# Kernel tuning notes

Hardware: AMD Instinct MI355X
Metric: run time of the kernel (lower is better)

Reference implementation:

```python
import jax, jax.numpy as jnp
import numpy as np

DMODEL = 2048
HEADS = 16
DHEAD = DMODEL // HEADS  # 128


def setup_inputs() -> dict:
    key = jax.random.key(0)
    ks = jax.random.split(key, 9)
    s = 0.02
    x = jax.random.normal(ks[0], (4, 2048, DMODEL), dtype=jnp.float32)
    Wq = jax.random.normal(ks[1], (DMODEL, DMODEL), dtype=jnp.float32) * s
    bq = jax.random.normal(ks[2], (DMODEL,), dtype=jnp.float32) * s
    Wk = jax.random.normal(ks[3], (DMODEL, DMODEL), dtype=jnp.float32) * s
    bk = jax.random.normal(ks[4], (DMODEL,), dtype=jnp.float32) * s
    Wv = jax.random.normal(ks[5], (DMODEL, DMODEL), dtype=jnp.float32) * s
    bv = jax.random.normal(ks[6], (DMODEL,), dtype=jnp.float32) * s
    Wo = jax.random.normal(ks[7], (DMODEL, DMODEL), dtype=jnp.float32) * s
    bo = jax.random.normal(ks[8], (DMODEL,), dtype=jnp.float32) * s
    return {"x": x, "Wq": Wq, "bq": bq, "Wk": Wk, "bk": bk, "Wv": Wv, "bv": bv, "Wo": Wo, "bo": bo}


def reference(x, Wq, bq, Wk, bk, Wv, bv, Wo, bo):
    b, l, _ = x.shape
    # projections: [b, l, dmodel] -> [b, l, heads, dhead]
    q = (x @ Wq + bq).reshape(b, l, HEADS, DHEAD)
    k = (x @ Wk + bk).reshape(b, l, HEADS, DHEAD)
    v = (x @ Wv + bv).reshape(b, l, HEADS, DHEAD)
    # NOTE: source applies 1/sqrt(dhead) twice -> total scale 1/dhead (faithful)
    a = jnp.einsum('blhd,bLhd->bhlL', q, k) * (1.0 / DHEAD)
    a = jax.nn.softmax(a, axis=-1)
    prefinal = jnp.einsum('bhlL,bLhd->blhd', a, v)
    out = prefinal.reshape(b, l, HEADS * DHEAD) @ Wo + bo
    return out
```

## Files before the change

kernel.cpp:

```cpp
#include <hip/hip_runtime.h>

#define DMODEL 2048
#define SEQ    2048
#define BATCH  4
#define HEADS  16
#define DHEAD  128

typedef __attribute__((ext_vector_type(8))) short short8;
typedef __attribute__((ext_vector_type(4))) float f32x4;
typedef __attribute__((ext_vector_type(16))) float f32x16;

__device__ __forceinline__ unsigned short f2bf(float f) {
  union { float f; unsigned u; } v; v.f = f;
  unsigned r = v.u + 0x7FFFu + ((v.u >> 16) & 1u);
  return (unsigned short)(r >> 16);
}

__global__ __launch_bounds__(256) void cvt_f32_bf16(const float* __restrict__ in,
                                                    unsigned short* __restrict__ out,
                                                    int n4) {
  int i = blockIdx.x * 256 + threadIdx.x;
  if (i >= n4) return;
  float4 v = ((const float4*)in)[i];
  ushort4 o;
  o.x = f2bf(v.x); o.y = f2bf(v.y); o.z = f2bf(v.z); o.w = f2bf(v.w);
  ((ushort4*)out)[i] = o;
}

__global__ __launch_bounds__(256) void transpose_cvt(const float* __restrict__ in,
                                                     unsigned short* __restrict__ out) {
  __shared__ float tile[32][33];
  const int tx = threadIdx.x, ty = threadIdx.y;
  const int x = blockIdx.x * 32 + tx;
  const int y0 = blockIdx.y * 32;
#pragma unroll
  for (int j = 0; j < 32; j += 8)
    tile[ty + j][tx] = in[(size_t)(y0 + ty + j) * DMODEL + x];
  __syncthreads();
  const int xo = blockIdx.y * 32 + tx;
  const int yo0 = blockIdx.x * 32;
#pragma unroll
  for (int j = 0; j < 32; j += 8)
    out[(size_t)(yo0 + ty + j) * DMODEL + xo] = f2bf(tile[tx][ty + j]);
}

__global__ __launch_bounds__(256) void transpose_v(const unsigned short* __restrict__ in,
                                                   unsigned short* __restrict__ out) {
  __shared__ unsigned short t[32][33];
  const int tx = threadIdx.x, ty = threadIdx.y;
  const int bid = blockIdx.x;
  const int lb = bid & 63;
  const int db = (bid >> 6) & 3;
  const int h  = (bid >> 8) & 15;
  const int b  = bid >> 12;
#pragma unroll
  for (int j = 0; j < 32; j += 8)
    t[ty + j][tx] = in[(size_t)(b * SEQ + lb * 32 + ty + j) * DMODEL + h * DHEAD + db * 32 + tx];
  __syncthreads();
  const size_t ob = ((size_t)(b * HEADS + h) * DHEAD + db * 32) * SEQ + lb * 32;
#pragma unroll
  for (int j = 0; j < 32; j += 8)
    out[ob + (size_t)(ty + j) * SEQ + tx] = t[tx][ty + j];
}

template <typename OUT_T, int NTN>
__global__ __launch_bounds__(512, 2) void gemm2(const unsigned short* __restrict__ A,
                                                const unsigned short* __restrict__ Bt,
                                                const float* __restrict__ b0,
                                                const float* __restrict__ b1,
                                                const float* __restrict__ b2,
                                                OUT_T* __restrict__ C) {
  __shared__ unsigned short As[2][256 * 64];
  __shared__ unsigned short Bs[2][256 * 64];

  const int tid = threadIdx.x;
  const int l = tid & 63, w = tid >> 6;
  const int wr = w >> 2, wc = w & 3;

  const int bid = blockIdx.x;
  const int q8 = (32 * NTN) >> 3;
  const int swz = (bid & 7) * q8 + (bid >> 3);
  const int tn = swz % NTN;
  const int tm = swz / NTN;

  const int srow = w * 8 + (l >> 3);
  const int schunk = (l & 7) ^ (l >> 3);
  const unsigned short* Ag = A + (size_t)(tm * 256 + srow) * DMODEL + schunk * 8;
  const unsigned short* Bg = Bt + (size_t)(tn * 256 + srow) * DMODEL + schunk * 8;

#define GLL(src, dst) __builtin_amdgcn_global_load_lds( \
    (const __attribute__((address_space(1))) void*)(src), \
    (__attribute__((address_space(3))) void*)(dst), 16, 0, 0)

#define STAGE(bf, kt) do { \
    GLL(Ag + (size_t)0 * 64 * DMODEL + (kt) * 64,   &As[bf][0 * 4096 + w * 512]); \
    GLL(Ag + (size_t)1 * 64 * DMODEL + (kt) * 64,   &As[bf][1 * 4096 + w * 512]); \
    GLL(Ag + (size_t)2 * 64 * DMODEL + (kt) * 64,   &As[bf][2 * 4096 + w * 512]); \
    GLL(Ag + (size_t)3 * 64 * DMODEL + (kt) * 64,   &As[bf][3 * 4096 + w * 512]); \
    GLL(Bg + (size_t)0 * 64 * DMODEL + (kt) * 64,   &Bs[bf][0 * 4096 + w * 512]); \
    GLL(Bg + (size_t)1 * 64 * DMODEL + (kt) * 64,   &Bs[bf][1 * 4096 + w * 512]); \
    GLL(Bg + (size_t)2 * 64 * DMODEL + (kt) * 64,   &Bs[bf][2 * 4096 + w * 512]); \
    GLL(Bg + (size_t)3 * 64 * DMODEL + (kt) * 64,   &Bs[bf][3 * 4096 + w * 512]); \
  } while (0)

  f32x4 acc[8][4] = {};

  STAGE(0, 0);
  int buf = 0;
  for (int t = 0; t < 32; ++t) {
    __builtin_amdgcn_s_barrier();
    __builtin_amdgcn_sched_barrier(0);
    if (t < 31) {
      STAGE(buf ^ 1, t + 1);
      __builtin_amdgcn_sched_barrier(0);
      asm volatile("s_waitcnt vmcnt(8)" ::: "memory");
    } else {
      asm volatile("s_waitcnt vmcnt(0)" ::: "memory");
    }
    __builtin_amdgcn_sched_barrier(0);
    __builtin_amdgcn_s_barrier();
    __builtin_amdgcn_sched_barrier(0);

    {
      const unsigned short* Asb = &As[buf][0];
      const unsigned short* Bsb = &Bs[buf][0];
      short8 bfr[4][2];
#pragma unroll
      for (int n = 0; n < 4; ++n) {
        const int row = wc * 64 + n * 16 + (l & 15);
#pragma unroll
        for (int ks = 0; ks < 2; ++ks)
          bfr[n][ks] = *(const short8*)&Bsb[row * 64 + (((ks * 4 + (l >> 4)) ^ (row & 7)) * 8)];
      }
      __builtin_amdgcn_s_setprio(1);
#pragma unroll
      for (int m = 0; m < 8; ++m) {
        const int row = wr * 128 + m * 16 + (l & 15);
        short8 af0 = *(const short8*)&Asb[row * 64 + (((0 + (l >> 4)) ^ (row & 7)) * 8)];
        short8 af1 = *(const short8*)&Asb[row * 64 + (((4 + (l >> 4)) ^ (row & 7)) * 8)];
#pragma unroll
        for (int n = 0; n < 4; ++n) {
          acc[m][n] = __builtin_amdgcn_mfma_f32_16x16x32_bf16(af0, bfr[n][0], acc[m][n], 0, 0, 0);
          acc[m][n] = __builtin_amdgcn_mfma_f32_16x16x32_bf16(af1, bfr[n][1], acc[m][n], 0, 0, 0);
        }
      }
      __builtin_amdgcn_s_setprio(0);
    }
    buf ^= 1;
  }
#undef STAGE
#undef GLL

  const int bsel = tn >> 3;
  const float* bp = (bsel == 0) ? b0 : ((bsel == 1) ? b1 : b2);
  OUT_T* Cb = C + (size_t)bsel * ((size_t)8192 * DMODEL);
  const int row0 = tm * 256 + wr * 128 + ((l >> 4) * 4);
  const int lc0 = (tn & 7) * 256 + wc * 64 + (l & 15);
#pragma unroll
  for (int n = 0; n < 4; ++n) {
    float bv = bp[lc0 + n * 16];
#pragma unroll
    for (int m = 0; m < 8; ++m) {
#pragma unroll
      for (int r = 0; r < 4; ++r) {
        float v = acc[m][n][r] + bv;
        size_t idx = (size_t)(row0 + m * 16 + r) * DMODEL + (lc0 + n * 16);
        if constexpr (sizeof(OUT_T) == 2) ((unsigned short*)Cb)[idx] = f2bf(v);
        else                              ((float*)Cb)[idx] = v;
      }
    }
  }
}

__global__ __launch_bounds__(256) void attn(const unsigned short* __restrict__ Q,
                                            const unsigned short* __restrict__ K,
                                            const unsigned short* __restrict__ V,
                                            unsigned short* __restrict__ O) {
  __shared__ unsigned short Ks[32 * 136];
  __shared__ unsigned short Vt[128 * 40];
  __shared__ unsigned short Ps[4][16 * 40];

  const int tid = threadIdx.x;
  const int l = tid & 63, w = tid >> 6;
  const int bh = blockIdx.x >> 5, qb = blockIdx.x & 31;
  const int b = bh >> 4, h = bh & 15;
  const size_t base = ((size_t)b * SEQ) * DMODEL + (size_t)h * DHEAD;

  const unsigned short* Qp = Q + base + (size_t)(qb * 64 + w * 16) * DMODEL;
  short8 qf[4];
#pragma unroll
  for (int dc = 0; dc < 4; ++dc)
    qf[dc] = *(const short8*)(Qp + (size_t)(l & 15) * DMODEL + dc * 32 + (l >> 4) * 8);

  f32x4 acc[8] = {};
  float sum[4] = {0.f, 0.f, 0.f, 0.f};

  const int skv = tid >> 3;
  const int sc = (tid & 7) * 16;
  const unsigned short* Kg = K + base + (size_t)skv * DMODEL + sc;
  const unsigned short* Vg = V + base + (size_t)skv * DMODEL + sc;

  const float cexp = 1.4426950408889634f / 128.0f;

  for (int kv0 = 0; kv0 < SEQ; kv0 += 32) {
    __syncthreads();
    short8 ka = *(const short8*)(Kg + (size_t)kv0 * DMODEL);
    short8 kb = *(const short8*)(Kg + (size_t)kv0 * DMODEL + 8);
    *(short8*)&Ks[skv * 136 + sc] = ka;
    *(short8*)&Ks[skv * 136 + sc + 8] = kb;
    short8 va = *(const short8*)(Vg + (size_t)kv0 * DMODEL);
    short8 vb = *(const short8*)(Vg + (size_t)kv0 * DMODEL + 8);
#pragma unroll
    for (int j = 0; j < 8; ++j) {
      Vt[(sc + j) * 40 + skv]     = (unsigned short)va[j];
      Vt[(sc + 8 + j) * 40 + skv] = (unsigned short)vb[j];
    }
    __syncthreads();

    f32x4 s[2];
#pragma unroll
    for (int nh = 0; nh < 2; ++nh) {
      f32x4 t = {};
#pragma unroll
      for (int dc = 0; dc < 4; ++dc) {
        short8 kf = *(const short8*)&Ks[(nh * 16 + (l & 15)) * 136 + dc * 32 + (l >> 4) * 8];
        t = __builtin_amdgcn_mfma_f32_16x16x32_bf16(qf[dc], kf, t, 0, 0, 0);
      }
      s[nh] = t;
    }

#pragma unroll
    for (int nh = 0; nh < 2; ++nh) {
#pragma unroll
      for (int r = 0; r < 4; ++r) {
        float p = exp2f(s[nh][r] * cexp);
        sum[r] += p;
        Ps[w][((l >> 4) * 4 + r) * 40 + (l & 15) + nh * 16] = f2bf(p);
      }
    }

    short8 pf = *(const short8*)&Ps[w][(l & 15) * 40 + (l >> 4) * 8];
#pragma unroll
    for (int db = 0; db < 8; ++db) {
      short8 vf = *(const short8*)&Vt[(db * 16 + (l & 15)) * 40 + (l >> 4) * 8];
      acc[db] = __builtin_amdgcn_mfma_f32_16x16x32_bf16(pf, vf, acc[db], 0, 0, 0);
    }
  }

  float inv[4];
#pragma unroll
  for (int r = 0; r < 4; ++r) {
    float s = sum[r];
    s += __shfl_xor(s, 1);
    s += __shfl_xor(s, 2);
    s += __shfl_xor(s, 4);
    s += __shfl_xor(s, 8);
    inv[r] = 1.0f / s;
  }
  unsigned short* Op = O + base + (size_t)(qb * 64 + w * 16) * DMODEL;
#pragma unroll
  for (int db = 0; db < 8; ++db)
#pragma unroll
    for (int r = 0; r < 4; ++r)
      Op[(size_t)((l >> 4) * 4 + r) * DMODEL + db * 16 + (l & 15)] = f2bf(acc[db][r] * inv[r]);
}

__global__ __launch_bounds__(256, 2) void attn6(const unsigned short* __restrict__ Q,
                                                const unsigned short* __restrict__ K,
                                                const unsigned short* __restrict__ VT,
                                                unsigned short* __restrict__ O) {
  __shared__ unsigned short Ks[2][64 * 128];
  __shared__ unsigned short Vs[2][128 * 64];

  const int tid = threadIdx.x;
  const int l = tid & 63, w = tid >> 6;
  const int x32 = l & 31, h = l >> 5;

  const int bid = blockIdx.x;
  const int swz = (bid & 7) * 64 + (bid >> 3);
  const int bh = swz >> 3, qb = swz & 7;
  const int b = bh >> 4, hh = bh & 15;
  const size_t base = ((size_t)b * SEQ) * DMODEL + (size_t)hh * DHEAD;
  const unsigned short* VTb = VT + (size_t)bh * DHEAD * SEQ;

  const unsigned short* Qp = Q + base + (size_t)(qb * 256 + w * 64) * DMODEL;
  short8 qfA[8], qfB[8];
#pragma unroll
  for (int dc = 0; dc < 8; ++dc) {
    qfA[dc] = *(const short8*)(Qp + (size_t)x32 * DMODEL + dc * 16 + h * 8);
    qfB[dc] = *(const short8*)(Qp + (size_t)(x32 + 32) * DMODEL + dc * 16 + h * 8);
  }

  const unsigned short* Kg0 = K + base + (size_t)(w * 16 + (l >> 4)) * DMODEL + (((l & 15) ^ (l >> 4)) * 8);
  const unsigned short* Kg1 = K + base + (size_t)(w * 16 + (l >> 4)) * DMODEL + (((l & 15) ^ ((l >> 4) + 4)) * 8);
  const unsigned short* Vg0 = VTb + (size_t)(w * 32 + (l >> 3)) * SEQ + (((l & 7) ^ (l >> 3)) * 8);

  unsigned short* KsD = &Ks[0][0];
  unsigned short* VsD = &Vs[0][0];

#define GLL(src, dst) __builtin_amdgcn_global_load_lds( \
    (const __attribute__((address_space(1))) void*)(src), \
    (__attribute__((address_space(3))) void*)(dst), 16, 0, 0)

#define STAGE(bf, kv0) do { \
    GLL(Kg0 + (size_t)(kv0) * DMODEL,        KsD + (bf) * 8192 + w * 2048 + 0 * 512); \
    GLL(Kg1 + (size_t)((kv0) + 4) * DMODEL,  KsD + (bf) * 8192 + w * 2048 + 1 * 512); \
    GLL(Kg0 + (size_t)((kv0) + 8) * DMODEL,  KsD + (bf) * 8192 + w * 2048 + 2 * 512); \
    GLL(Kg1 + (size_t)((kv0) + 12) * DMODEL, KsD + (bf) * 8192 + w * 2048 + 3 * 512); \
    GLL(Vg0 + (size_t)0 * SEQ + (kv0),       VsD + (bf) * 8192 + w * 2048 + 0 * 512); \
    GLL(Vg0 + (size_t)8 * SEQ + (kv0),       VsD + (bf) * 8192 + w * 2048 + 1 * 512); \
    GLL(Vg0 + (size_t)16 * SEQ + (kv0),      VsD + (bf) * 8192 + w * 2048 + 2 * 512); \
    GLL(Vg0 + (size_t)24 * SEQ + (kv0),      VsD + (bf) * 8192 + w * 2048 + 3 * 512); \
  } while (0)

  f32x16 acc0[4] = {}, acc1[4] = {};
  float sum0 = 0.f, sum1 = 0.f;
  const float cexp = 1.4426950408889634f / 128.0f;

#define COMPUTE_SUB(bf, s) do { \
    const unsigned short* Kb_ = &Ks[bf][(s) * 32 * 128]; \
    const unsigned short* Vb_ = &Vs[bf][0]; \
    f32x16 sa0 = {}, sa1 = {}; \
    __builtin_amdgcn_s_setprio(1); \
    _Pragma("unroll") \
    for (int dc = 0; dc < 8; ++dc) { \
      short8 kf = *(const short8*)&Kb_[x32 * 128 + (((dc * 2 + h) ^ (x32 & 7)) * 8)]; \
      sa0 = __builtin_amdgcn_mfma_f32_32x32x16_bf16(kf, qfA[dc], sa0, 0, 0, 0); \
      sa1 = __builtin_amdgcn_mfma_f32_32x32x16_bf16(kf, qfB[dc], sa1, 0, 0, 0); \
    } \
    __builtin_amdgcn_s_setprio(0); \
    union { unsigned u[4]; short8 s8; } pf0A, pf1A, pf0B, pf1B; \
    { \
      float p[16]; \
      _Pragma("unroll") \
      for (int r = 0; r < 16; ++r) { p[r] = __builtin_amdgcn_exp2f(sa0[r] * cexp); sum0 += p[r]; } \
      unsigned pk0[4], pk1[4]; \
      _Pragma("unroll") \
      for (int blk = 0; blk < 4; ++blk) { \
        asm("v_cvt_pk_bf16_f32 %0, %1, %2" : "=v"(pk0[blk]) : "v"(p[blk * 4 + 0]), "v"(p[blk * 4 + 1])); \
        asm("v_cvt_pk_bf16_f32 %0, %1, %2" : "=v"(pk1[blk]) : "v"(p[blk * 4 + 2]), "v"(p[blk * 4 + 3])); \
      } \
      unsigned a0 = pk0[0], a1 = pk0[1], b0 = pk1[0], b1 = pk1[1]; \
      asm("v_permlane32_swap_b32 %0, %1" : "+v"(a0), "+v"(a1)); \
      asm("v_permlane32_swap_b32 %0, %1" : "+v"(b0), "+v"(b1)); \
      pf0A.u[0] = a0; pf0A.u[1] = b0; pf0A.u[2] = a1; pf0A.u[3] = b1; \
      unsigned c0 = pk0[2], c1 = pk0[3], d0 = pk1[2], d1 = pk1[3]; \
      asm("v_permlane32_swap_b32 %0, %1" : "+v"(c0), "+v"(c1)); \
      asm("v_permlane32_swap_b32 %0, %1" : "+v"(d0), "+v"(d1)); \
      pf1A.u[0] = c0; pf1A.u[1] = d0; pf1A.u[2] = c1; pf1A.u[3] = d1; \
    } \
    { \
      float p[16]; \
      _Pragma("unroll") \
      for (int r = 0; r < 16; ++r) { p[r] = __builtin_amdgcn_exp2f(sa1[r] * cexp); sum1 += p[r]; } \
      unsigned pk0[4], pk1[4]; \
      _Pragma("unroll") \
      for (int blk = 0; blk < 4; ++blk) { \
        asm("v_cvt_pk_bf16_f32 %0, %1, %2" : "=v"(pk0[blk]) : "v"(p[blk * 4 + 0]), "v"(p[blk * 4 + 1])); \
        asm("v_cvt_pk_bf16_f32 %0, %1, %2" : "=v"(pk1[blk]) : "v"(p[blk * 4 + 2]), "v"(p[blk * 4 + 3])); \
      } \
      unsigned a0 = pk0[0], a1 = pk0[1], b0 = pk1[0], b1 = pk1[1]; \
      asm("v_permlane32_swap_b32 %0, %1" : "+v"(a0), "+v"(a1)); \
      asm("v_permlane32_swap_b32 %0, %1" : "+v"(b0), "+v"(b1)); \
      pf0B.u[0] = a0; pf0B.u[1] = b0; pf0B.u[2] = a1; pf0B.u[3] = b1; \
      unsigned c0 = pk0[2], c1 = pk0[3], d0 = pk1[2], d1 = pk1[3]; \
      asm("v_permlane32_swap_b32 %0, %1" : "+v"(c0), "+v"(c1)); \
      asm("v_permlane32_swap_b32 %0, %1" : "+v"(d0), "+v"(d1)); \
      pf1B.u[0] = c0; pf1B.u[1] = d0; pf1B.u[2] = c1; pf1B.u[3] = d1; \
    } \
    __builtin_amdgcn_s_setprio(1); \
    _Pragma("unroll") \
    for (int db = 0; db < 4; ++db) { \
      const int row = db * 32 + x32; \
      short8 vf0 = *(const short8*)&Vb_[row * 64 + ((((s) * 4 + 0 + h) ^ (row & 7)) * 8)]; \
      short8 vf1 = *(const short8*)&Vb_[row * 64 + ((((s) * 4 + 2 + h) ^ (row & 7)) * 8)]; \
      acc0[db] = __builtin_amdgcn_mfma_f32_32x32x16_bf16(pf0A.s8, vf0, acc0[db], 0, 0, 0); \
      acc1[db] = __builtin_amdgcn_mfma_f32_32x32x16_bf16(pf0B.s8, vf0, acc1[db], 0, 0, 0); \
      acc0[db] = __builtin_amdgcn_mfma_f32_32x32x16_bf16(pf1A.s8, vf1, acc0[db], 0, 0, 0); \
      acc1[db] = __builtin_amdgcn_mfma_f32_32x32x16_bf16(pf1B.s8, vf1, acc1[db], 0, 0, 0); \
    } \
    __builtin_amdgcn_s_setprio(0); \
  } while (0)

  STAGE(0, 0);
  int buf = 0;
  for (int t = 0; t < 32; ++t) {
    __builtin_amdgcn_s_barrier();
    __builtin_amdgcn_sched_barrier(0);
    if (t < 31) {
      STAGE(buf ^ 1, (t + 1) * 64);
      __builtin_amdgcn_sched_barrier(0);
      asm volatile("s_waitcnt vmcnt(8)" ::: "memory");
    } else {
      asm volatile("s_waitcnt vmcnt(0)" ::: "memory");
    }
    __builtin_amdgcn_sched_barrier(0);
    __builtin_amdgcn_s_barrier();
    __builtin_amdgcn_sched_barrier(0);
    COMPUTE_SUB(buf, 0);
    COMPUTE_SUB(buf, 1);
    buf ^= 1;
  }
#undef COMPUTE_SUB
#undef STAGE
#undef GLL

  sum0 += __shfl_xor(sum0, 32);
  sum1 += __shfl_xor(sum1, 32);
  float inv0 = 1.0f / sum0;
  float inv1 = 1.0f / sum1;
  float invq0[16], invq1[16];
#pragma unroll
  for (int r = 0; r < 16; ++r) {
    const int crow = (r & 3) + 8 * (r >> 2) + 4 * h;
    invq0[r] = __shfl(inv0, crow);
    invq1[r] = __shfl(inv1, crow);
  }

  unsigned short* Op = O + base + (size_t)(qb * 256 + w * 64) * DMODEL;
#pragma unroll
  for (int db = 0; db < 4; ++db)
#pragma unroll
    for (int r = 0; r < 16; ++r) {
      const int crow = (r & 3) + 8 * (r >> 2) + 4 * h;
      Op[(size_t)crow * DMODEL + db * 32 + x32] = f2bf(acc0[db][r] * invq0[r]);
      Op[(size_t)(crow + 32) * DMODEL + db * 32 + x32] = f2bf(acc1[db][r] * invq1[r]);
    }
}

extern "C" void kernel_launch(void* const* d_in, const int* in_sizes, int n_in,
                              void* d_out, int out_size, void* d_ws, size_t ws_size,
                              hipStream_t stream) {
  const float* x  = (const float*)d_in[0];
  const float* Wq = (const float*)d_in[1];
  const float* bq = (const float*)d_in[2];
  const float* Wk = (const float*)d_in[3];
  const float* bk = (const float*)d_in[4];
  const float* Wv = (const float*)d_in[5];
  const float* bv = (const float*)d_in[6];
  const float* Wo = (const float*)d_in[7];
  const float* bo = (const float*)d_in[8];

  char* ws = (char*)d_ws;
  unsigned short* xb  = (unsigned short*)ws;
  unsigned short* WqT = (unsigned short*)(ws + 33554432);
  unsigned short* WkT = (unsigned short*)(ws + 41943040);
  unsigned short* WvT = (unsigned short*)(ws + 50331648);
  unsigned short* WoT = (unsigned short*)(ws + 58720256);
  unsigned short* Qb  = (unsigned short*)(ws + 67108864);
  unsigned short* Kb  = (unsigned short*)(ws + 100663296);
  unsigned short* Vb  = (unsigned short*)(ws + 134217728);
  unsigned short* VTg = (unsigned short*)(ws + 167772160);
  unsigned short* Pf  = xb;

  const bool vt_ok = (ws_size >= (size_t)201326592);

  cvt_f32_bf16<<<16384, 256, 0, stream>>>(x, xb, (BATCH * SEQ * DMODEL) / 4);

  dim3 tb(32, 8), tg(64, 64);
  transpose_cvt<<<tg, tb, 0, stream>>>(Wq, WqT);
  transpose_cvt<<<tg, tb, 0, stream>>>(Wk, WkT);
  transpose_cvt<<<tg, tb, 0, stream>>>(Wv, WvT);
  transpose_cvt<<<tg, tb, 0, stream>>>(Wo, WoT);

  gemm2<unsigned short, 24><<<768, 512, 0, stream>>>(xb, WqT, bq, bk, bv, Qb);

  if (vt_ok) {
    transpose_v<<<16384, dim3(32, 8), 0, stream>>>(Vb, VTg);
    attn6<<<512, 256, 0, stream>>>(Qb, Kb, VTg, Pf);
  } else {
    attn<<<2048, 256, 0, stream>>>(Qb, Kb, Vb, Pf);
  }

  gemm2<float, 8><<<256, 512, 0, stream>>>(Pf, WoT, bo, bo, bo, (float*)d_out);
}
```

Before: 529.6 us.

## Halve GEMM K-tile to raise occupancy and merge weight transposes into one launch

The projection GEMM's K-step drops from 64 to 32, which halves LDS use per block (64KB to 32KB). The launch bound rises to 4 blocks per CU, the global-to-LDS staging and XOR swizzle are reworked for 32-wide rows, and the loop runs 64 iterations instead of 32. The four weight transpose-convert launches are folded into one kernel indexed by blockIdx.z. The intent is better occupancy and latency hiding plus less launch overhead. In exchange there are twice as many barriers per K, and the 4-block bound may force register spills with the 128 accumulator floats.

```diff
diff --git a/kernel.cpp b/kernel.cpp
--- a/kernel.cpp
+++ b/kernel.cpp
@@ -27,9 +27,18 @@
   ((ushort4*)out)[i] = o;
 }
 
-__global__ __launch_bounds__(256) void transpose_cvt(const float* __restrict__ in,
-                                                     unsigned short* __restrict__ out) {
+__global__ __launch_bounds__(256) void transpose_cvt4(const float* __restrict__ w0,
+                                                      const float* __restrict__ w1,
+                                                      const float* __restrict__ w2,
+                                                      const float* __restrict__ w3,
+                                                      unsigned short* __restrict__ o0,
+                                                      unsigned short* __restrict__ o1,
+                                                      unsigned short* __restrict__ o2,
+                                                      unsigned short* __restrict__ o3) {
   __shared__ float tile[32][33];
+  const int z = blockIdx.z;
+  const float* in = (z == 0) ? w0 : (z == 1) ? w1 : (z == 2) ? w2 : w3;
+  unsigned short* out = (z == 0) ? o0 : (z == 1) ? o1 : (z == 2) ? o2 : o3;
   const int tx = threadIdx.x, ty = threadIdx.y;
   const int x = blockIdx.x * 32 + tx;
   const int y0 = blockIdx.y * 32;
@@ -64,14 +73,14 @@
 }
 
 template <typename OUT_T, int NTN>
-__global__ __launch_bounds__(512, 2) void gemm2(const unsigned short* __restrict__ A,
+__global__ __launch_bounds__(512, 4) void gemm3(const unsigned short* __restrict__ A,
                                                 const unsigned short* __restrict__ Bt,
                                                 const float* __restrict__ b0,
                                                 const float* __restrict__ b1,
                                                 const float* __restrict__ b2,
                                                 OUT_T* __restrict__ C) {
-  __shared__ unsigned short As[2][256 * 64];
-  __shared__ unsigned short Bs[2][256 * 64];
+  __shared__ unsigned short As[2][256 * 32];
+  __shared__ unsigned short Bs[2][256 * 32];
 
   const int tid = threadIdx.x;
   const int l = tid & 63, w = tid >> 6;
@@ -83,37 +92,36 @@
   const int tn = swz % NTN;
   const int tm = swz / NTN;
 
-  const int srow = w * 8 + (l >> 3);
-  const int schunk = (l & 7) ^ (l >> 3);
-  const unsigned short* Ag = A + (size_t)(tm * 256 + srow) * DMODEL + schunk * 8;
-  const unsigned short* Bg = Bt + (size_t)(tn * 256 + srow) * DMODEL + schunk * 8;
+  const int srow = tid >> 2;
+  const int schunk = (tid & 3) ^ ((tid >> 3) & 3);
+  const unsigned short* Ag0 = A + (size_t)(tm * 256 + srow) * DMODEL + schunk * 8;
+  const unsigned short* Ag1 = Ag0 + (size_t)128 * DMODEL;
+  const unsigned short* Bg0 = Bt + (size_t)(tn * 256 + srow) * DMODEL + schunk * 8;
+  const unsigned short* Bg1 = Bg0 + (size_t)128 * DMODEL;
 
 #define GLL(src, dst) __builtin_amdgcn_global_load_lds( \
     (const __attribute__((address_space(1))) void*)(src), \
     (__attribute__((address_space(3))) void*)(dst), 16, 0, 0)
 
 #define STAGE(bf, kt) do { \
-    GLL(Ag + (size_t)0 * 64 * DMODEL + (kt) * 64,   &As[bf][0 * 4096 + w * 512]); \
-    GLL(Ag + (size_t)1 * 64 * DMODEL + (kt) * 64,   &As[bf][1 * 4096 + w * 512]); \
-    GLL(Ag + (size_t)2 * 64 * DMODEL + (kt) * 64,   &As[bf][2 * 4096 + w * 512]); \
-    GLL(Ag + (size_t)3 * 64 * DMODEL + (kt) * 64,   &As[bf][3 * 4096 + w * 512]); \
-    GLL(Bg + (size_t)0 * 64 * DMODEL + (kt) * 64,   &Bs[bf][0 * 4096 + w * 512]); \
-    GLL(Bg + (size_t)1 * 64 * DMODEL + (kt) * 64,   &Bs[bf][1 * 4096 + w * 512]); \
-    GLL(Bg + (size_t)2 * 64 * DMODEL + (kt) * 64,   &Bs[bf][2 * 4096 + w * 512]); \
-    GLL(Bg + (size_t)3 * 64 * DMODEL + (kt) * 64,   &Bs[bf][3 * 4096 + w * 512]); \
+    GLL(Ag0 + (kt) * 32, &As[bf][0 * 4096 + w * 512]); \
+    GLL(Ag1 + (kt) * 32, &As[bf][1 * 4096 + w * 512]); \
+    GLL(Bg0 + (kt) * 32, &Bs[bf][0 * 4096 + w * 512]); \
+    GLL(Bg1 + (kt) * 32, &Bs[bf][1 * 4096 + w * 512]); \
   } while (0)
 
   f32x4 acc[8][4] = {};
+  const int rchunk = ((l >> 4) ^ (((l & 15) >> 1) & 3)) * 8;
 
   STAGE(0, 0);
   int buf = 0;
-  for (int t = 0; t < 32; ++t) {
+  for (int t = 0; t < 64; ++t) {
     __builtin_amdgcn_s_barrier();
     __builtin_amdgcn_sched_barrier(0);
-    if (t < 31) {
+    if (t < 63) {
       STAGE(buf ^ 1, t + 1);
       __builtin_amdgcn_sched_barrier(0);
-      asm volatile("s_waitcnt vmcnt(8)" ::: "memory");
+      asm volatile("s_waitcnt vmcnt(4)" ::: "memory");
     } else {
       asm volatile("s_waitcnt vmcnt(0)" ::: "memory");
     }
@@ -124,25 +132,20 @@
     {
       const unsigned short* Asb = &As[buf][0];
       const unsigned short* Bsb = &Bs[buf][0];
-      short8 bfr[4][2];
+      short8 bfr[4];
 #pragma unroll
       for (int n = 0; n < 4; ++n) {
         const int row = wc * 64 + n * 16 + (l & 15);
-#pragma unroll
-        for (int ks = 0; ks < 2; ++ks)
-          bfr[n][ks] = *(const short8*)&Bsb[row * 64 + (((ks * 4 + (l >> 4)) ^ (row & 7)) * 8)];
+        bfr[n] = *(const short8*)&Bsb[row * 32 + rchunk];
       }
       __builtin_amdgcn_s_setprio(1);
 #pragma unroll
       for (int m = 0; m < 8; ++m) {
         const int row = wr * 128 + m * 16 + (l & 15);
-        short8 af0 = *(const short8*)&Asb[row * 64 + (((0 + (l >> 4)) ^ (row & 7)) * 8)];
-        short8 af1 = *(const short8*)&Asb[row * 64 + (((4 + (l >> 4)) ^ (row & 7)) * 8)];
-#pragma unroll
-        for (int n = 0; n < 4; ++n) {
-          acc[m][n] = __builtin_amdgcn_mfma_f32_16x16x32_bf16(af0, bfr[n][0], acc[m][n], 0, 0, 0);
-          acc[m][n] = __builtin_amdgcn_mfma_f32_16x16x32_bf16(af1, bfr[n][1], acc[m][n], 0, 0, 0);
-        }
+        short8 af = *(const short8*)&Asb[row * 32 + rchunk];
+#pragma unroll
+        for (int n = 0; n < 4; ++n)
+          acc[m][n] = __builtin_amdgcn_mfma_f32_16x16x32_bf16(af, bfr[n], acc[m][n], 0, 0, 0);
       }
       __builtin_amdgcn_s_setprio(0);
     }
@@ -457,13 +460,9 @@
 
   cvt_f32_bf16<<<16384, 256, 0, stream>>>(x, xb, (BATCH * SEQ * DMODEL) / 4);
 
-  dim3 tb(32, 8), tg(64, 64);
-  transpose_cvt<<<tg, tb, 0, stream>>>(Wq, WqT);
-  transpose_cvt<<<tg, tb, 0, stream>>>(Wk, WkT);
-  transpose_cvt<<<tg, tb, 0, stream>>>(Wv, WvT);
-  transpose_cvt<<<tg, tb, 0, stream>>>(Wo, WoT);
-
-  gemm2<unsigned short, 24><<<768, 512, 0, stream>>>(xb, WqT, bq, bk, bv, Qb);
+  transpose_cvt4<<<dim3(64, 64, 4), dim3(32, 8), 0, stream>>>(Wq, Wk, Wv, Wo, WqT, WkT, WvT, WoT);
+
+  gemm3<unsigned short, 24><<<768, 512, 0, stream>>>(xb, WqT, bq, bk, bv, Qb);
 
   if (vt_ok) {
     transpose_v<<<16384, dim3(32, 8), 0, stream>>>(Vb, VTg);
@@ -472,5 +471,5 @@
     attn<<<2048, 256, 0, stream>>>(Qb, Kb, Vb, Pf);
   }
 
-  gemm2<float, 8><<<256, 512, 0, stream>>>(Pf, WoT, bo, bo, bo, (float*)d_out);
-}
+  gemm3<float, 8><<<256, 512, 0, stream>>>(Pf, WoT, bo, bo, bo, (float*)d_out);
+}
```

After: 1.787 ms. +237.4%, slower.

## Split fused QKV GEMM into three launches and batch weight transposes

Applied to the files above, without the earlier changes.

Replaces the single 768-block fused QKV projection GEMM, which used a grouped tile swizzle, with three separate 256-block GEMM launches that share a simpler tile mapping without the swizzle. It also merges the four weight transpose-convert launches into one launch, with the grid z dimension selecting which weight matrix each block handles. The merge removes launch overhead. Splitting the QKV GEMM loses the single large grid and the L2-friendly swizzle, so each launch may fill the GPU poorly and reuse cache less.

```diff
diff --git a/kernel.cpp b/kernel.cpp
--- a/kernel.cpp
+++ b/kernel.cpp
@@ -27,9 +27,18 @@
   ((ushort4*)out)[i] = o;
 }
 
-__global__ __launch_bounds__(256) void transpose_cvt(const float* __restrict__ in,
-                                                     unsigned short* __restrict__ out) {
+__global__ __launch_bounds__(256) void transpose_cvt4(const float* __restrict__ w0,
+                                                      const float* __restrict__ w1,
+                                                      const float* __restrict__ w2,
+                                                      const float* __restrict__ w3,
+                                                      unsigned short* __restrict__ o0,
+                                                      unsigned short* __restrict__ o1,
+                                                      unsigned short* __restrict__ o2,
+                                                      unsigned short* __restrict__ o3) {
   __shared__ float tile[32][33];
+  const int z = blockIdx.z;
+  const float* in = (z == 0) ? w0 : (z == 1) ? w1 : (z == 2) ? w2 : w3;
+  unsigned short* out = (z == 0) ? o0 : (z == 1) ? o1 : (z == 2) ? o2 : o3;
   const int tx = threadIdx.x, ty = threadIdx.y;
   const int x = blockIdx.x * 32 + tx;
   const int y0 = blockIdx.y * 32;
@@ -63,12 +72,10 @@
     out[ob + (size_t)(ty + j) * SEQ + tx] = t[tx][ty + j];
 }
 
-template <typename OUT_T, int NTN>
+template <typename OUT_T>
 __global__ __launch_bounds__(512, 2) void gemm2(const unsigned short* __restrict__ A,
                                                 const unsigned short* __restrict__ Bt,
-                                                const float* __restrict__ b0,
-                                                const float* __restrict__ b1,
-                                                const float* __restrict__ b2,
+                                                const float* __restrict__ bias,
                                                 OUT_T* __restrict__ C) {
   __shared__ unsigned short As[2][256 * 64];
   __shared__ unsigned short Bs[2][256 * 64];
@@ -78,10 +85,8 @@
   const int wr = w >> 2, wc = w & 3;
 
   const int bid = blockIdx.x;
-  const int q8 = (32 * NTN) >> 3;
-  const int swz = (bid & 7) * q8 + (bid >> 3);
-  const int tn = swz % NTN;
-  const int tm = swz / NTN;
+  const int tn = bid & 7;
+  const int tm = bid >> 3;
 
   const int srow = w * 8 + (l >> 3);
   const int schunk = (l & 7) ^ (l >> 3);
@@ -151,22 +156,19 @@
 #undef STAGE
 #undef GLL
 
-  const int bsel = tn >> 3;
-  const float* bp = (bsel == 0) ? b0 : ((bsel == 1) ? b1 : b2);
-  OUT_T* Cb = C + (size_t)bsel * ((size_t)8192 * DMODEL);
   const int row0 = tm * 256 + wr * 128 + ((l >> 4) * 4);
-  const int lc0 = (tn & 7) * 256 + wc * 64 + (l & 15);
+  const int col0 = tn * 256 + wc * 64 + (l & 15);
 #pragma unroll
   for (int n = 0; n < 4; ++n) {
-    float bv = bp[lc0 + n * 16];
+    float bv = bias[col0 + n * 16];
 #pragma unroll
     for (int m = 0; m < 8; ++m) {
 #pragma unroll
       for (int r = 0; r < 4; ++r) {
         float v = acc[m][n][r] + bv;
-        size_t idx = (size_t)(row0 + m * 16 + r) * DMODEL + (lc0 + n * 16);
-        if constexpr (sizeof(OUT_T) == 2) ((unsigned short*)Cb)[idx] = f2bf(v);
-        else                              ((float*)Cb)[idx] = v;
+        size_t idx = (size_t)(row0 + m * 16 + r) * DMODEL + (col0 + n * 16);
+        if constexpr (sizeof(OUT_T) == 2) ((unsigned short*)C)[idx] = f2bf(v);
+        else                              ((float*)C)[idx] = v;
       }
     }
   }
@@ -457,13 +459,11 @@
 
   cvt_f32_bf16<<<16384, 256, 0, stream>>>(x, xb, (BATCH * SEQ * DMODEL) / 4);
 
-  dim3 tb(32, 8), tg(64, 64);
-  transpose_cvt<<<tg, tb, 0, stream>>>(Wq, WqT);
-  transpose_cvt<<<tg, tb, 0, stream>>>(Wk, WkT);
-  transpose_cvt<<<tg, tb, 0, stream>>>(Wv, WvT);
-  transpose_cvt<<<tg, tb, 0, stream>>>(Wo, WoT);
-
-  gemm2<unsigned short, 24><<<768, 512, 0, stream>>>(xb, WqT, bq, bk, bv, Qb);
+  transpose_cvt4<<<dim3(64, 64, 4), dim3(32, 8), 0, stream>>>(Wq, Wk, Wv, Wo, WqT, WkT, WvT, WoT);
+
+  gemm2<unsigned short><<<256, 512, 0, stream>>>(xb, WqT, bq, Qb);
+  gemm2<unsigned short><<<256, 512, 0, stream>>>(xb, WkT, bk, Kb);
+  gemm2<unsigned short><<<256, 512, 0, stream>>>(xb, WvT, bv, Vb);
 
   if (vt_ok) {
     transpose_v<<<16384, dim3(32, 8), 0, stream>>>(Vb, VTg);
@@ -472,5 +472,5 @@
     attn<<<2048, 256, 0, stream>>>(Qb, Kb, Vb, Pf);
   }
 
-  gemm2<float, 8><<<256, 512, 0, stream>>>(Pf, WoT, bo, bo, bo, (float*)d_out);
-}
+  gemm2<float><<<256, 512, 0, stream>>>(Pf, WoT, bo, (float*)d_out);
+}
```

After: 579.9 us. 9.5% more time.

## Split GEMM A/B staging, double-buffer A fragments, batch weight transposes

Applied to the files above, without the earlier changes.

The GEMM main loop now issues the next tile's A loads at the top of the iteration and defers the B loads into the middle of the MFMA loop. It also register-double-buffers A fragments so LDS reads for the next 32-row slice overlap the current MFMAs. The goal is better overlap of global-to-LDS traffic and LDS reads with matrix-core work, at the cost of more registers and a tighter vmcnt dependency. Separately, the four weight transpose launches are merged into one launch with a z-dimension to cut launch overhead.

```diff
diff --git a/kernel.cpp b/kernel.cpp
--- a/kernel.cpp
+++ b/kernel.cpp
@@ -27,9 +27,18 @@
   ((ushort4*)out)[i] = o;
 }
 
-__global__ __launch_bounds__(256) void transpose_cvt(const float* __restrict__ in,
-                                                     unsigned short* __restrict__ out) {
+__global__ __launch_bounds__(256) void transpose_cvt4(const float* __restrict__ w0,
+                                                      const float* __restrict__ w1,
+                                                      const float* __restrict__ w2,
+                                                      const float* __restrict__ w3,
+                                                      unsigned short* __restrict__ o0,
+                                                      unsigned short* __restrict__ o1,
+                                                      unsigned short* __restrict__ o2,
+                                                      unsigned short* __restrict__ o3) {
   __shared__ float tile[32][33];
+  const int z = blockIdx.z;
+  const float* in = (z == 0) ? w0 : (z == 1) ? w1 : (z == 2) ? w2 : w3;
+  unsigned short* out = (z == 0) ? o0 : (z == 1) ? o1 : (z == 2) ? o2 : o3;
   const int tx = threadIdx.x, ty = threadIdx.y;
   const int x = blockIdx.x * 32 + tx;
   const int y0 = blockIdx.y * 32;
@@ -92,11 +101,13 @@
     (const __attribute__((address_space(1))) void*)(src), \
     (__attribute__((address_space(3))) void*)(dst), 16, 0, 0)
 
-#define STAGE(bf, kt) do { \
+#define STAGE_A(bf, kt) do { \
     GLL(Ag + (size_t)0 * 64 * DMODEL + (kt) * 64,   &As[bf][0 * 4096 + w * 512]); \
     GLL(Ag + (size_t)1 * 64 * DMODEL + (kt) * 64,   &As[bf][1 * 4096 + w * 512]); \
     GLL(Ag + (size_t)2 * 64 * DMODEL + (kt) * 64,   &As[bf][2 * 4096 + w * 512]); \
     GLL(Ag + (size_t)3 * 64 * DMODEL + (kt) * 64,   &As[bf][3 * 4096 + w * 512]); \
+  } while (0)
+#define STAGE_B(bf, kt) do { \
     GLL(Bg + (size_t)0 * 64 * DMODEL + (kt) * 64,   &Bs[bf][0 * 4096 + w * 512]); \
     GLL(Bg + (size_t)1 * 64 * DMODEL + (kt) * 64,   &Bs[bf][1 * 4096 + w * 512]); \
     GLL(Bg + (size_t)2 * 64 * DMODEL + (kt) * 64,   &Bs[bf][2 * 4096 + w * 512]); \
@@ -105,15 +116,16 @@
 
   f32x4 acc[8][4] = {};
 
-  STAGE(0, 0);
+  STAGE_A(0, 0);
+  STAGE_B(0, 0);
   int buf = 0;
   for (int t = 0; t < 32; ++t) {
     __builtin_amdgcn_s_barrier();
     __builtin_amdgcn_sched_barrier(0);
     if (t < 31) {
-      STAGE(buf ^ 1, t + 1);
+      STAGE_A(buf ^ 1, t + 1);
       __builtin_amdgcn_sched_barrier(0);
-      asm volatile("s_waitcnt vmcnt(8)" ::: "memory");
+      asm volatile("s_waitcnt vmcnt(4)" ::: "memory");
     } else {
       asm volatile("s_waitcnt vmcnt(0)" ::: "memory");
     }
@@ -132,23 +144,41 @@
         for (int ks = 0; ks < 2; ++ks)
           bfr[n][ks] = *(const short8*)&Bsb[row * 64 + (((ks * 4 + (l >> 4)) ^ (row & 7)) * 8)];
       }
-      __builtin_amdgcn_s_setprio(1);
-#pragma unroll
-      for (int m = 0; m < 8; ++m) {
-        const int row = wr * 128 + m * 16 + (l & 15);
-        short8 af0 = *(const short8*)&Asb[row * 64 + (((0 + (l >> 4)) ^ (row & 7)) * 8)];
-        short8 af1 = *(const short8*)&Asb[row * 64 + (((4 + (l >> 4)) ^ (row & 7)) * 8)];
-#pragma unroll
-        for (int n = 0; n < 4; ++n) {
-          acc[m][n] = __builtin_amdgcn_mfma_f32_16x16x32_bf16(af0, bfr[n][0], acc[m][n], 0, 0, 0);
-          acc[m][n] = __builtin_amdgcn_mfma_f32_16x16x32_bf16(af1, bfr[n][1], acc[m][n], 0, 0, 0);
+      short8 af[2][2][2];
+#pragma unroll
+      for (int mi = 0; mi < 2; ++mi) {
+        const int row = wr * 128 + mi * 16 + (l & 15);
+        af[0][mi][0] = *(const short8*)&Asb[row * 64 + (((0 + (l >> 4)) ^ (row & 7)) * 8)];
+        af[0][mi][1] = *(const short8*)&Asb[row * 64 + (((4 + (l >> 4)) ^ (row & 7)) * 8)];
+      }
+#pragma unroll
+      for (int p = 0; p < 4; ++p) {
+        const int cur = p & 1, nxt = cur ^ 1;
+        if (p < 3) {
+#pragma unroll
+          for (int mi = 0; mi < 2; ++mi) {
+            const int row = wr * 128 + (p + 1) * 32 + mi * 16 + (l & 15);
+            af[nxt][mi][0] = *(const short8*)&Asb[row * 64 + (((0 + (l >> 4)) ^ (row & 7)) * 8)];
+            af[nxt][mi][1] = *(const short8*)&Asb[row * 64 + (((4 + (l >> 4)) ^ (row & 7)) * 8)];
+          }
         }
+        if (p == 2 && t < 31) STAGE_B(buf ^ 1, t + 1);
+        __builtin_amdgcn_s_setprio(1);
+#pragma unroll
+        for (int mi = 0; mi < 2; ++mi) {
+#pragma unroll
+          for (int n = 0; n < 4; ++n) {
+            acc[p * 2 + mi][n] = __builtin_amdgcn_mfma_f32_16x16x32_bf16(af[cur][mi][0], bfr[n][0], acc[p * 2 + mi][n], 0, 0, 0);
+            acc[p * 2 + mi][n] = __builtin_amdgcn_mfma_f32_16x16x32_bf16(af[cur][mi][1], bfr[n][1], acc[p * 2 + mi][n], 0, 0, 0);
+          }
+        }
+        __builtin_amdgcn_s_setprio(0);
       }
-      __builtin_amdgcn_s_setprio(0);
     }
     buf ^= 1;
   }
-#undef STAGE
+#undef STAGE_A
+#undef STAGE_B
 #undef GLL
 
   const int bsel = tn >> 3;
@@ -457,11 +487,7 @@
 
   cvt_f32_bf16<<<16384, 256, 0, stream>>>(x, xb, (BATCH * SEQ * DMODEL) / 4);
 
-  dim3 tb(32, 8), tg(64, 64);
-  transpose_cvt<<<tg, tb, 0, stream>>>(Wq, WqT);
-  transpose_cvt<<<tg, tb, 0, stream>>>(Wk, WkT);
-  transpose_cvt<<<tg, tb, 0, stream>>>(Wv, WvT);
-  transpose_cvt<<<tg, tb, 0, stream>>>(Wo, WoT);
+  transpose_cvt4<<<dim3(64, 64, 4), dim3(32, 8), 0, stream>>>(Wq, Wk, Wv, Wo, WqT, WkT, WvT, WoT);
 
   gemm2<unsigned short, 24><<<768, 512, 0, stream>>>(xb, WqT, bq, bk, bv, Qb);
 
```

After: 503.5 us. 4.9% less time.
